# Kernel tuning notes

Hardware: AMD Instinct MI355X
Metric: run time of the kernel (lower is better)

The kernel has to match this reference:

```python
import jax, jax.numpy as jnp
import numpy as np

IN_C = 256
OUT_C = 256
HID = IN_C * 2
N_POINTS = 262144
N_NODES = 8192
B = 16
MAX_NODES = 512
EPS = 1e-5


def _mlp(h, w1, b1, g1, be1, w2, b2):
    # PyG MLP([C, 2C, out], norm='layer_norm'): lin -> layernorm -> relu -> (dropout, eval=identity) -> lin
    h = h @ w1 + b1
    mu = jnp.mean(h, axis=-1, keepdims=True)
    var = jnp.var(h, axis=-1, keepdims=True)
    h = (h - mu) * jax.lax.rsqrt(var + EPS) * g1 + be1
    h = jax.nn.relu(h)
    return h @ w2 + b2


def setup_inputs() -> dict:
    key = jax.random.key(0)
    ks = jax.random.split(key, 16)
    x = jax.random.normal(ks[0], (N_POINTS, IN_C), dtype=jnp.float32)
    f_point_batches = jnp.sort(jax.random.randint(ks[1], (N_POINTS,), 0, N_NODES)).astype(jnp.int32)
    # equal-sized graphs (16 graphs x 512 nodes), sorted as torch.split/pad_sequence assume
    g_node_batches = jnp.repeat(jnp.arange(B, dtype=jnp.int32), MAX_NODES)
    s = 1.0 / np.sqrt(IN_C)
    s2 = 1.0 / np.sqrt(HID)
    def lin(k, fan_in, shape, scale):
        return jax.random.uniform(k, shape, jnp.float32, -scale, scale)
    params = {}
    for i, name in enumerate(['Wq', 'Wk']):
        base = 2 + i * 6
        params[f'{name}_w1'] = lin(ks[base + 0], IN_C, (IN_C, HID), s)
        params[f'{name}_b1'] = lin(ks[base + 1], IN_C, (HID,), s)
        params[f'{name}_g1'] = jnp.ones((HID,), jnp.float32)
        params[f'{name}_be1'] = jnp.zeros((HID,), jnp.float32)
        params[f'{name}_w2'] = lin(ks[base + 2], HID, (HID, OUT_C), s2)
        params[f'{name}_b2'] = lin(ks[base + 3], HID, (OUT_C,), s2)
    return dict(x=x, f_point_batches=f_point_batches, g_node_batches=g_node_batches,
                num_graphs=B, max_nodes=MAX_NODES, **params)


def reference(x, f_point_batches, g_node_batches, num_graphs, max_nodes,
              Wq_w1, Wq_b1, Wq_g1, Wq_be1, Wq_w2, Wq_b2,
              Wk_w1, Wk_b1, Wk_g1, Wk_be1, Wk_w2, Wk_b2):
    n_nodes = g_node_batches.shape[0]
    C = x.shape[1]
    # scatter_mean over points -> per-node feature means [n_nodes, C]
    sums = jax.ops.segment_sum(x, f_point_batches, num_segments=n_nodes)
    cnt = jax.ops.segment_sum(jnp.ones((x.shape[0],), x.dtype), f_point_batches, num_segments=n_nodes)
    mean = sums / jnp.maximum(cnt, 1.0)[:, None]
    # ragged split by graph + pad_sequence -> [B, max_nodes, C]
    starts = jnp.searchsorted(g_node_batches, jnp.arange(num_graphs, dtype=g_node_batches.dtype))
    pos = jnp.arange(n_nodes) - starts[g_node_batches]
    padded = jnp.zeros((num_graphs, max_nodes, C), x.dtype).at[g_node_batches, pos].set(mean, mode='drop')
    q = _mlp(padded, Wq_w1, Wq_b1, Wq_g1, Wq_be1, Wq_w2, Wq_b2)  # [B, MAXN, out]
    k = _mlp(padded, Wk_w1, Wk_b1, Wk_g1, Wk_be1, Wk_w2, Wk_b2)
    return jnp.einsum('bnd,bmd->bnm', q, k)  # bmm(q, k^T)
```

## Files before the change

### kernel.cpp

```cpp
#include <hip/hip_runtime.h>
#include <hip/hip_bf16.h>

#define N_POINTS 262144
#define N_NODES  8192
#define IN_C     256
#define HID      512
#define OUT_C    256
#define NB       16
#define MAXN     512
#define EPSV     1e-5f
#define NPB      32

typedef __attribute__((ext_vector_type(8))) short short8;
typedef __attribute__((ext_vector_type(4))) float f32x4;
typedef __attribute__((ext_vector_type(4))) float f4v;
#define MFMA16(a, b, c) __builtin_amdgcn_mfma_f32_16x16x32_bf16((a), (b), (c), 0, 0, 0)


__global__ __launch_bounds__(256) void prelude_k(
    const int* __restrict__ fpb, int* __restrict__ starts,
    const float* __restrict__ W1q, const float* __restrict__ W1k,
    const float* __restrict__ W2q, const float* __restrict__ W2k,
    __hip_bfloat16* __restrict__ P1q, __hip_bfloat16* __restrict__ P1k,
    __hip_bfloat16* __restrict__ P2q, __hip_bfloat16* __restrict__ P2k)
{
  if (blockIdx.x < 1024) {
    const int i = blockIdx.x * 256 + threadIdx.x;
    const int cur = fpb[i];
    const int prev = (i == 0) ? -1 : fpb[i - 1];
    for (int n = prev + 1; n <= cur; ++n) starts[n] = i;
    if (i == N_POINTS - 1)
      for (int n = cur + 1; n <= N_NODES; ++n) starts[n] = N_POINTS;
    return;
  }
  const int bid = blockIdx.x - 1024;
  const int sel = bid >> 6;
  const float* W; __hip_bfloat16* P; int N;
  switch (sel) {
    case 0:  W = W1q; P = P1q; N = HID;   break;
    case 1:  W = W1k; P = P1k; N = HID;   break;
    case 2:  W = W2q; P = P2q; N = OUT_C; break;
    default: W = W2k; P = P2k; N = OUT_C; break;
  }
  const int idx = (bid & 63) * 256 + threadIdx.x;
  const int NF = N >> 4;
  const int lane = idx & 63;
  const int nf = (idx >> 6) % NF;
  const int ks = idx / (64 * NF);
  const int k0 = ks * 32 + (lane >> 4) * 8;
  const int n  = nf * 16 + (lane & 15);
  __hip_bfloat16 tmp[8];
  #pragma unroll
  for (int j = 0; j < 8; ++j) tmp[j] = __float2bfloat16(W[(size_t)(k0 + j) * N + n]);
  *(uint4*)(P + (size_t)idx * 8) = *(uint4*)tmp;
}

__global__ __launch_bounds__(512, 2) void fused_mlp_k(
    const float* __restrict__ x, const int* __restrict__ starts,
    const __hip_bfloat16* __restrict__ P1q, const __hip_bfloat16* __restrict__ P2q,
    const float* __restrict__ b1q, const float* __restrict__ g1q,
    const float* __restrict__ be1q, const float* __restrict__ b2q,
    const __hip_bfloat16* __restrict__ P1k, const __hip_bfloat16* __restrict__ P2k,
    const float* __restrict__ b1k, const float* __restrict__ g1k,
    const float* __restrict__ be1k, const float* __restrict__ b2k,
    __hip_bfloat16* __restrict__ qo, __hip_bfloat16* __restrict__ ko)
{
  const int n0 = blockIdx.x * NPB;
  const int t = threadIdx.x;
  const int w = t >> 6, l = t & 63, lg = l >> 4, lm = l & 15;
  const int h = w >> 2;
  const int c = w & 3;

  const __hip_bfloat16* P1 = h ? P1k : P1q;
  const __hip_bfloat16* P2 = h ? P2k : P2q;
  const float* b1  = h ? b1k  : b1q;
  const float* g1  = h ? g1k  : g1q;
  const float* be1 = h ? be1k : be1q;
  const float* b2  = h ? b2k  : b2q;
  __hip_bfloat16* out = h ? ko : qo;

  __shared__ __hip_bfloat16 As[NPB * 264];
  __shared__ __hip_bfloat16 Hs[2][NPB * 520];
  __shared__ float lnp[8][NPB][2];

  #pragma unroll
  for (int i = 0; i < 4; ++i) {
    const int nl = w * 4 + i;
    const int node = n0 + nl;
    const int s_ = starts[node], e_ = starts[node + 1];
    const int cnt = e_ - s_;
    f4v a0 = (f4v)0.f, a1 = (f4v)0.f, a2 = (f4v)0.f, a3 = (f4v)0.f, a4 = (f4v)0.f, a5 = (f4v)0.f;
    if (cnt > 0) {
      for (int r = s_; r < e_; r += 6) {
        int i0 = r,     i1 = r + 1, i2 = r + 2, i3 = r + 3, i4 = r + 4, i5 = r + 5;
        int v1ok = i1 < e_, v2ok = i2 < e_, v3ok = i3 < e_, v4ok = i4 < e_, v5ok = i5 < e_;
        i1 = v1ok ? i1 : s_; i2 = v2ok ? i2 : s_; i3 = v3ok ? i3 : s_;
        i4 = v4ok ? i4 : s_; i5 = v5ok ? i5 : s_;
        f4v v0 = __builtin_nontemporal_load((const f4v*)(x + (size_t)i0 * IN_C + l * 4));
        f4v v1 = __builtin_nontemporal_load((const f4v*)(x + (size_t)i1 * IN_C + l * 4));
        f4v v2 = __builtin_nontemporal_load((const f4v*)(x + (size_t)i2 * IN_C + l * 4));
        f4v v3 = __builtin_nontemporal_load((const f4v*)(x + (size_t)i3 * IN_C + l * 4));
        f4v v4 = __builtin_nontemporal_load((const f4v*)(x + (size_t)i4 * IN_C + l * 4));
        f4v v5 = __builtin_nontemporal_load((const f4v*)(x + (size_t)i5 * IN_C + l * 4));
        a0 += v0;
        a1 += v1ok ? v1 : (f4v)0.f;
        a2 += v2ok ? v2 : (f4v)0.f;
        a3 += v3ok ? v3 : (f4v)0.f;
        a4 += v4ok ? v4 : (f4v)0.f;
        a5 += v5ok ? v5 : (f4v)0.f;
      }
    }
    a0 += a1 + a2 + a3 + a4 + a5;
    const float inv = cnt > 0 ? 1.0f / (float)cnt : 0.0f;
    __hip_bfloat16 o[4];
    o[0] = __float2bfloat16(a0.x * inv);
    o[1] = __float2bfloat16(a0.y * inv);
    o[2] = __float2bfloat16(a0.z * inv);
    o[3] = __float2bfloat16(a0.w * inv);
    *(uint2*)(As + nl * 264 + l * 4) = *(uint2*)o;
  }
  __syncthreads();

  f32x4 acc1[2][8];
  #pragma unroll
  for (int mi = 0; mi < 2; ++mi)
    #pragma unroll
    for (int nj = 0; nj < 8; ++nj)
      #pragma unroll
      for (int r = 0; r < 4; ++r) acc1[mi][nj][r] = 0.f;

  for (int ks = 0; ks < 8; ++ks) {
    short8 a0 = *(const short8*)(As + lm * 264 + ks * 32 + lg * 8);
    short8 a1 = *(const short8*)(As + (16 + lm) * 264 + ks * 32 + lg * 8);
    const __hip_bfloat16* bp = P1 + ((size_t)(ks * 32 + c * 8) * 64 + l) * 8;
    #pragma unroll
    for (int nj = 0; nj < 8; ++nj) {
      short8 b = *(const short8*)(bp + (size_t)nj * 512);
      acc1[0][nj] = MFMA16(a0, b, acc1[0][nj]);
      acc1[1][nj] = MFMA16(a1, b, acc1[1][nj]);
    }
  }

  float b1v[8], g1v[8], e1v[8];
  #pragma unroll
  for (int nj = 0; nj < 8; ++nj) {
    const int col = c * 128 + nj * 16 + lm;
    b1v[nj] = b1[col]; g1v[nj] = g1[col]; e1v[nj] = be1[col];
  }
  #pragma unroll
  for (int mi = 0; mi < 2; ++mi)
    #pragma unroll
    for (int nj = 0; nj < 8; ++nj)
      #pragma unroll
      for (int r = 0; r < 4; ++r) acc1[mi][nj][r] += b1v[nj];

  #pragma unroll
  for (int mi = 0; mi < 2; ++mi)
    #pragma unroll
    for (int r = 0; r < 4; ++r) {
      float s = 0.f, q = 0.f;
      #pragma unroll
      for (int nj = 0; nj < 8; ++nj) {
        const float v = acc1[mi][nj][r];
        s += v; q += v * v;
      }
      #pragma unroll
      for (int off = 1; off < 16; off <<= 1) {
        s += __shfl_xor(s, off);
        q += __shfl_xor(q, off);
      }
      if (lm == 0) {
        const int row = mi * 16 + lg * 4 + r;
        lnp[w][row][0] = s;
        lnp[w][row][1] = q;
      }
    }
  __syncthreads();

  #pragma unroll
  for (int mi = 0; mi < 2; ++mi)
    #pragma unroll
    for (int r = 0; r < 4; ++r) {
      const int row = mi * 16 + lg * 4 + r;
      float S = 0.f, Q = 0.f;
      #pragma unroll
      for (int w2 = 0; w2 < 4; ++w2) {
        S += lnp[h * 4 + w2][row][0];
        Q += lnp[h * 4 + w2][row][1];
      }
      const float mu = S * (1.0f / HID);
      const float rs = rsqrtf(Q * (1.0f / HID) - mu * mu + EPSV);
      #pragma unroll
      for (int nj = 0; nj < 8; ++nj) {
        const float y = (acc1[mi][nj][r] - mu) * rs * g1v[nj] + e1v[nj];
        Hs[h][row * 520 + c * 128 + nj * 16 + lm] = __float2bfloat16(fmaxf(y, 0.f));
      }
    }
  __syncthreads();

  f32x4 acc2[2][4];
  #pragma unroll
  for (int mi = 0; mi < 2; ++mi)
    #pragma unroll
    for (int nj = 0; nj < 4; ++nj)
      #pragma unroll
      for (int r = 0; r < 4; ++r) acc2[mi][nj][r] = 0.f;

  for (int ks = 0; ks < 16; ++ks) {
    short8 a0 = *(const short8*)(Hs[h] + lm * 520 + ks * 32 + lg * 8);
    short8 a1 = *(const short8*)(Hs[h] + (16 + lm) * 520 + ks * 32 + lg * 8);
    const __hip_bfloat16* bp = P2 + ((size_t)(ks * 16 + c * 4) * 64 + l) * 8;
    #pragma unroll
    for (int nj = 0; nj < 4; ++nj) {
      short8 b = *(const short8*)(bp + (size_t)nj * 512);
      acc2[0][nj] = MFMA16(a0, b, acc2[0][nj]);
      acc2[1][nj] = MFMA16(a1, b, acc2[1][nj]);
    }
  }

  float b2v[4];
  #pragma unroll
  for (int nj = 0; nj < 4; ++nj) b2v[nj] = b2[c * 64 + nj * 16 + lm];
  #pragma unroll
  for (int mi = 0; mi < 2; ++mi)
    #pragma unroll
    for (int nj = 0; nj < 4; ++nj)
      #pragma unroll
      for (int r = 0; r < 4; ++r) {
        const int row = n0 + mi * 16 + lg * 4 + r;
        const int col = c * 64 + nj * 16 + lm;
        out[(size_t)row * OUT_C + col] = __float2bfloat16(acc2[mi][nj][r] + b2v[nj]);
      }
}

__global__ __launch_bounds__(256, 4) void bmm_k(
    const __hip_bfloat16* __restrict__ q, const __hip_bfloat16* __restrict__ k,
    float* __restrict__ out)
{
  const int b  = blockIdx.z;
  const int n0 = blockIdx.x * 64;
  const int m0 = blockIdx.y * 64;
  const int t = threadIdx.x;
  const int w = t >> 6, l = t & 63, lg = l >> 4, lm = l & 15;

  const __hip_bfloat16* qb = q + ((size_t)b * MAXN + n0 + w * 16) * OUT_C;
  const __hip_bfloat16* kb = k + ((size_t)b * MAXN + m0) * OUT_C;

  f32x4 acc[4];
  #pragma unroll
  for (int nj = 0; nj < 4; ++nj)
    #pragma unroll
    for (int r = 0; r < 4; ++r) acc[nj][r] = 0.f;

  for (int ks = 0; ks < 8; ++ks) {
    short8 a = *(const short8*)(qb + (size_t)lm * OUT_C + ks * 32 + lg * 8);
    #pragma unroll
    for (int nj = 0; nj < 4; ++nj) {
      short8 bb = *(const short8*)(kb + (size_t)(nj * 16 + lm) * OUT_C + ks * 32 + lg * 8);
      acc[nj] = MFMA16(a, bb, acc[nj]);
    }
  }

  #pragma unroll
  for (int nj = 0; nj < 4; ++nj)
    #pragma unroll
    for (int r = 0; r < 4; ++r) {
      const int nrow = n0 + w * 16 + lg * 4 + r;
      const int mcol = m0 + nj * 16 + lm;
      out[((size_t)b * MAXN + nrow) * MAXN + mcol] = acc[nj][r];
    }
}

extern "C" void kernel_launch(void* const* d_in, const int* in_sizes, int n_in,
                              void* d_out, int out_size, void* d_ws, size_t ws_size,
                              hipStream_t stream)
{
  const float* x   = (const float*)d_in[0];
  const int*   fpb = (const int*)d_in[1];
  const float* Wq_w1  = (const float*)d_in[5];
  const float* Wq_b1  = (const float*)d_in[6];
  const float* Wq_g1  = (const float*)d_in[7];
  const float* Wq_be1 = (const float*)d_in[8];
  const float* Wq_w2  = (const float*)d_in[9];
  const float* Wq_b2  = (const float*)d_in[10];
  const float* Wk_w1  = (const float*)d_in[11];
  const float* Wk_b1  = (const float*)d_in[12];
  const float* Wk_g1  = (const float*)d_in[13];
  const float* Wk_be1 = (const float*)d_in[14];
  const float* Wk_w2  = (const float*)d_in[15];
  const float* Wk_b2  = (const float*)d_in[16];

  __hip_bfloat16* ws = (__hip_bfloat16*)d_ws;
  __hip_bfloat16* P1q  = ws;
  __hip_bfloat16* P1k  = P1q + 131072;
  __hip_bfloat16* P2q  = P1k + 131072;
  __hip_bfloat16* P2k  = P2q + 131072;
  __hip_bfloat16* qo   = P2k + 131072;
  __hip_bfloat16* ko   = qo + 2097152;
  int* starts = (int*)(ko + 2097152);
  float* out = (float*)d_out;

  prelude_k<<<1280, 256, 0, stream>>>(fpb, starts,
      Wq_w1, Wk_w1, Wq_w2, Wk_w2, P1q, P1k, P2q, P2k);
  fused_mlp_k<<<N_NODES / NPB, 512, 0, stream>>>(
      x, starts, P1q, P2q, Wq_b1, Wq_g1, Wq_be1, Wq_b2,
      P1k, P2k, Wk_b1, Wk_g1, Wk_be1, Wk_b2, qo, ko);
  bmm_k<<<dim3(8, 8, NB), 256, 0, stream>>>(qo, ko, out);
}
```

Before: 92.66 us.

## Serialize Q and K MLP heads across all waves to raise occupancy

Instead of splitting the 8 waves into a Q group and a K group, all 8 waves now process the Q MLP and then the K MLP in sequence. Each wave holds half as many accumulators and the block keeps only one hidden buffer in shared memory, and the launch bound goes from 2 to 4 blocks per CU. The scatter-mean loop is also rewritten as a plain 4-way unrolled loop with a scalar tail, replacing the 6-way predicated non-temporal loads. In exchange the MLP phases run serially, with extra barriers and a second pass of the layernorm reduction.

```diff
diff --git a/kernel.cpp b/kernel.cpp
--- a/kernel.cpp
+++ b/kernel.cpp
@@ -55,7 +55,23 @@
   *(uint4*)(P + (size_t)idx * 8) = *(uint4*)tmp;
 }
 
-__global__ __launch_bounds__(512, 2) void fused_mlp_k(
+__device__ __forceinline__ void accum_rows(
+    const float* __restrict__ x, int lo, int hi, int l,
+    f4v& a0, f4v& a1, f4v& a2, f4v& a3)
+{
+  int r = lo;
+  for (; r + 4 <= hi; r += 4) {
+    f4v v0 = *(const f4v*)(x + (size_t)(r + 0) * IN_C + l * 4);
+    f4v v1 = *(const f4v*)(x + (size_t)(r + 1) * IN_C + l * 4);
+    f4v v2 = *(const f4v*)(x + (size_t)(r + 2) * IN_C + l * 4);
+    f4v v3 = *(const f4v*)(x + (size_t)(r + 3) * IN_C + l * 4);
+    a0 += v0; a1 += v1; a2 += v2; a3 += v3;
+  }
+  for (; r < hi; ++r)
+    a0 += *(const f4v*)(x + (size_t)r * IN_C + l * 4);
+}
+
+__global__ __launch_bounds__(512, 4) void fused_mlp_k(
     const float* __restrict__ x, const int* __restrict__ starts,
     const __hip_bfloat16* __restrict__ P1q, const __hip_bfloat16* __restrict__ P2q,
     const float* __restrict__ b1q, const float* __restrict__ g1q,
@@ -68,19 +84,9 @@
   const int n0 = blockIdx.x * NPB;
   const int t = threadIdx.x;
   const int w = t >> 6, l = t & 63, lg = l >> 4, lm = l & 15;
-  const int h = w >> 2;
-  const int c = w & 3;
-
-  const __hip_bfloat16* P1 = h ? P1k : P1q;
-  const __hip_bfloat16* P2 = h ? P2k : P2q;
-  const float* b1  = h ? b1k  : b1q;
-  const float* g1  = h ? g1k  : g1q;
-  const float* be1 = h ? be1k : be1q;
-  const float* b2  = h ? b2k  : b2q;
-  __hip_bfloat16* out = h ? ko : qo;
 
   __shared__ __hip_bfloat16 As[NPB * 264];
-  __shared__ __hip_bfloat16 Hs[2][NPB * 520];
+  __shared__ __hip_bfloat16 Hs[NPB * 520];
   __shared__ float lnp[8][NPB][2];
 
   #pragma unroll
@@ -88,29 +94,10 @@
     const int nl = w * 4 + i;
     const int node = n0 + nl;
     const int s_ = starts[node], e_ = starts[node + 1];
+    f4v a0 = (f4v)0.f, a1 = (f4v)0.f, a2 = (f4v)0.f, a3 = (f4v)0.f;
+    accum_rows(x, s_, e_, l, a0, a1, a2, a3);
+    a0 += a1 + a2 + a3;
     const int cnt = e_ - s_;
-    f4v a0 = (f4v)0.f, a1 = (f4v)0.f, a2 = (f4v)0.f, a3 = (f4v)0.f, a4 = (f4v)0.f, a5 = (f4v)0.f;
-    if (cnt > 0) {
-      for (int r = s_; r < e_; r += 6) {
-        int i0 = r,     i1 = r + 1, i2 = r + 2, i3 = r + 3, i4 = r + 4, i5 = r + 5;
-        int v1ok = i1 < e_, v2ok = i2 < e_, v3ok = i3 < e_, v4ok = i4 < e_, v5ok = i5 < e_;
-        i1 = v1ok ? i1 : s_; i2 = v2ok ? i2 : s_; i3 = v3ok ? i3 : s_;
-        i4 = v4ok ? i4 : s_; i5 = v5ok ? i5 : s_;
-        f4v v0 = __builtin_nontemporal_load((const f4v*)(x + (size_t)i0 * IN_C + l * 4));
-        f4v v1 = __builtin_nontemporal_load((const f4v*)(x + (size_t)i1 * IN_C + l * 4));
-        f4v v2 = __builtin_nontemporal_load((const f4v*)(x + (size_t)i2 * IN_C + l * 4));
-        f4v v3 = __builtin_nontemporal_load((const f4v*)(x + (size_t)i3 * IN_C + l * 4));
-        f4v v4 = __builtin_nontemporal_load((const f4v*)(x + (size_t)i4 * IN_C + l * 4));
-        f4v v5 = __builtin_nontemporal_load((const f4v*)(x + (size_t)i5 * IN_C + l * 4));
-        a0 += v0;
-        a1 += v1ok ? v1 : (f4v)0.f;
-        a2 += v2ok ? v2 : (f4v)0.f;
-        a3 += v3ok ? v3 : (f4v)0.f;
-        a4 += v4ok ? v4 : (f4v)0.f;
-        a5 += v5ok ? v5 : (f4v)0.f;
-      }
-    }
-    a0 += a1 + a2 + a3 + a4 + a5;
     const float inv = cnt > 0 ? 1.0f / (float)cnt : 0.0f;
     __hip_bfloat16 o[4];
     o[0] = __float2bfloat16(a0.x * inv);
@@ -121,116 +108,127 @@
   }
   __syncthreads();
 
-  f32x4 acc1[2][8];
-  #pragma unroll
-  for (int mi = 0; mi < 2; ++mi)
-    #pragma unroll
-    for (int nj = 0; nj < 8; ++nj)
-      #pragma unroll
-      for (int r = 0; r < 4; ++r) acc1[mi][nj][r] = 0.f;
-
-  for (int ks = 0; ks < 8; ++ks) {
-    short8 a0 = *(const short8*)(As + lm * 264 + ks * 32 + lg * 8);
-    short8 a1 = *(const short8*)(As + (16 + lm) * 264 + ks * 32 + lg * 8);
-    const __hip_bfloat16* bp = P1 + ((size_t)(ks * 32 + c * 8) * 64 + l) * 8;
-    #pragma unroll
-    for (int nj = 0; nj < 8; ++nj) {
-      short8 b = *(const short8*)(bp + (size_t)nj * 512);
-      acc1[0][nj] = MFMA16(a0, b, acc1[0][nj]);
-      acc1[1][nj] = MFMA16(a1, b, acc1[1][nj]);
-    }
-  }
-
-  float b1v[8], g1v[8], e1v[8];
-  #pragma unroll
-  for (int nj = 0; nj < 8; ++nj) {
-    const int col = c * 128 + nj * 16 + lm;
-    b1v[nj] = b1[col]; g1v[nj] = g1[col]; e1v[nj] = be1[col];
-  }
-  #pragma unroll
-  for (int mi = 0; mi < 2; ++mi)
-    #pragma unroll
-    for (int nj = 0; nj < 8; ++nj)
-      #pragma unroll
-      for (int r = 0; r < 4; ++r) acc1[mi][nj][r] += b1v[nj];
-
-  #pragma unroll
-  for (int mi = 0; mi < 2; ++mi)
-    #pragma unroll
-    for (int r = 0; r < 4; ++r) {
-      float s = 0.f, q = 0.f;
-      #pragma unroll
-      for (int nj = 0; nj < 8; ++nj) {
-        const float v = acc1[mi][nj][r];
-        s += v; q += v * v;
+  for (int hh = 0; hh < 2; ++hh) {
+    const __hip_bfloat16* P1 = hh ? P1k : P1q;
+    const __hip_bfloat16* P2 = hh ? P2k : P2q;
+    const float* b1  = hh ? b1k  : b1q;
+    const float* g1  = hh ? g1k  : g1q;
+    const float* be1 = hh ? be1k : be1q;
+    const float* b2  = hh ? b2k  : b2q;
+    __hip_bfloat16* out = hh ? ko : qo;
+
+    f32x4 acc1[2][4];
+    #pragma unroll
+    for (int mi = 0; mi < 2; ++mi)
+      #pragma unroll
+      for (int nj = 0; nj < 4; ++nj)
+        #pragma unroll
+        for (int r = 0; r < 4; ++r) acc1[mi][nj][r] = 0.f;
+
+    for (int ks = 0; ks < 8; ++ks) {
+      short8 a0 = *(const short8*)(As + lm * 264 + ks * 32 + lg * 8);
+      short8 a1 = *(const short8*)(As + (16 + lm) * 264 + ks * 32 + lg * 8);
+      const __hip_bfloat16* bp = P1 + ((size_t)(ks * 32 + w * 4) * 64 + l) * 8;
+      #pragma unroll
+      for (int nj = 0; nj < 4; ++nj) {
+        short8 b = *(const short8*)(bp + (size_t)nj * 512);
+        acc1[0][nj] = MFMA16(a0, b, acc1[0][nj]);
+        acc1[1][nj] = MFMA16(a1, b, acc1[1][nj]);
       }
-      #pragma unroll
-      for (int off = 1; off < 16; off <<= 1) {
-        s += __shfl_xor(s, off);
-        q += __shfl_xor(q, off);
+    }
+
+    float b1v[4], g1v[4], e1v[4];
+    #pragma unroll
+    for (int nj = 0; nj < 4; ++nj) {
+      const int col = w * 64 + nj * 16 + lm;
+      b1v[nj] = b1[col]; g1v[nj] = g1[col]; e1v[nj] = be1[col];
+    }
+    #pragma unroll
+    for (int mi = 0; mi < 2; ++mi)
+      #pragma unroll
+      for (int nj = 0; nj < 4; ++nj)
+        #pragma unroll
+        for (int r = 0; r < 4; ++r) acc1[mi][nj][r] += b1v[nj];
+
+    #pragma unroll
+    for (int mi = 0; mi < 2; ++mi)
+      #pragma unroll
+      for (int r = 0; r < 4; ++r) {
+        float s = 0.f, q = 0.f;
+        #pragma unroll
+        for (int nj = 0; nj < 4; ++nj) {
+          const float v = acc1[mi][nj][r];
+          s += v; q += v * v;
+        }
+        #pragma unroll
+        for (int off = 1; off < 16; off <<= 1) {
+          s += __shfl_xor(s, off);
+          q += __shfl_xor(q, off);
+        }
+        if (lm == 0) {
+          const int row = mi * 16 + lg * 4 + r;
+          lnp[w][row][0] = s;
+          lnp[w][row][1] = q;
+        }
       }
-      if (lm == 0) {
+    __syncthreads();
+
+    #pragma unroll
+    for (int mi = 0; mi < 2; ++mi)
+      #pragma unroll
+      for (int r = 0; r < 4; ++r) {
         const int row = mi * 16 + lg * 4 + r;
-        lnp[w][row][0] = s;
-        lnp[w][row][1] = q;
+        float S = 0.f, Q = 0.f;
+        #pragma unroll
+        for (int w2 = 0; w2 < 8; ++w2) {
+          S += lnp[w2][row][0];
+          Q += lnp[w2][row][1];
+        }
+        const float mu = S * (1.0f / HID);
+        const float rs = rsqrtf(Q * (1.0f / HID) - mu * mu + EPSV);
+        #pragma unroll
+        for (int nj = 0; nj < 4; ++nj) {
+          const float y = (acc1[mi][nj][r] - mu) * rs * g1v[nj] + e1v[nj];
+          Hs[row * 520 + w * 64 + nj * 16 + lm] = __float2bfloat16(fmaxf(y, 0.f));
+        }
       }
-    }
-  __syncthreads();
-
-  #pragma unroll
-  for (int mi = 0; mi < 2; ++mi)
-    #pragma unroll
-    for (int r = 0; r < 4; ++r) {
-      const int row = mi * 16 + lg * 4 + r;
-      float S = 0.f, Q = 0.f;
-      #pragma unroll
-      for (int w2 = 0; w2 < 4; ++w2) {
-        S += lnp[h * 4 + w2][row][0];
-        Q += lnp[h * 4 + w2][row][1];
+    __syncthreads();
+
+    f32x4 acc2[2][2];
+    #pragma unroll
+    for (int mi = 0; mi < 2; ++mi)
+      #pragma unroll
+      for (int nj = 0; nj < 2; ++nj)
+        #pragma unroll
+        for (int r = 0; r < 4; ++r) acc2[mi][nj][r] = 0.f;
+
+    for (int ks = 0; ks < 16; ++ks) {
+      short8 a0 = *(const short8*)(Hs + lm * 520 + ks * 32 + lg * 8);
+      short8 a1 = *(const short8*)(Hs + (16 + lm) * 520 + ks * 32 + lg * 8);
+      const __hip_bfloat16* bp = P2 + ((size_t)(ks * 16 + w * 2) * 64 + l) * 8;
+      #pragma unroll
+      for (int nj = 0; nj < 2; ++nj) {
+        short8 b = *(const short8*)(bp + (size_t)nj * 512);
+        acc2[0][nj] = MFMA16(a0, b, acc2[0][nj]);
+        acc2[1][nj] = MFMA16(a1, b, acc2[1][nj]);
       }
-      const float mu = S * (1.0f / HID);
-      const float rs = rsqrtf(Q * (1.0f / HID) - mu * mu + EPSV);
-      #pragma unroll
-      for (int nj = 0; nj < 8; ++nj) {
-        const float y = (acc1[mi][nj][r] - mu) * rs * g1v[nj] + e1v[nj];
-        Hs[h][row * 520 + c * 128 + nj * 16 + lm] = __float2bfloat16(fmaxf(y, 0.f));
-      }
-    }
-  __syncthreads();
-
-  f32x4 acc2[2][4];
-  #pragma unroll
-  for (int mi = 0; mi < 2; ++mi)
-    #pragma unroll
-    for (int nj = 0; nj < 4; ++nj)
-      #pragma unroll
-      for (int r = 0; r < 4; ++r) acc2[mi][nj][r] = 0.f;
-
-  for (int ks = 0; ks < 16; ++ks) {
-    short8 a0 = *(const short8*)(Hs[h] + lm * 520 + ks * 32 + lg * 8);
-    short8 a1 = *(const short8*)(Hs[h] + (16 + lm) * 520 + ks * 32 + lg * 8);
-    const __hip_bfloat16* bp = P2 + ((size_t)(ks * 16 + c * 4) * 64 + l) * 8;
-    #pragma unroll
-    for (int nj = 0; nj < 4; ++nj) {
-      short8 b = *(const short8*)(bp + (size_t)nj * 512);
-      acc2[0][nj] = MFMA16(a0, b, acc2[0][nj]);
-      acc2[1][nj] = MFMA16(a1, b, acc2[1][nj]);
-    }
-  }
-
-  float b2v[4];
-  #pragma unroll
-  for (int nj = 0; nj < 4; ++nj) b2v[nj] = b2[c * 64 + nj * 16 + lm];
-  #pragma unroll
-  for (int mi = 0; mi < 2; ++mi)
-    #pragma unroll
-    for (int nj = 0; nj < 4; ++nj)
-      #pragma unroll
-      for (int r = 0; r < 4; ++r) {
-        const int row = n0 + mi * 16 + lg * 4 + r;
-        const int col = c * 64 + nj * 16 + lm;
-        out[(size_t)row * OUT_C + col] = __float2bfloat16(acc2[mi][nj][r] + b2v[nj]);
-      }
+    }
+
+    float b2v[2];
+    #pragma unroll
+    for (int nj = 0; nj < 2; ++nj) b2v[nj] = b2[w * 32 + nj * 16 + lm];
+    #pragma unroll
+    for (int mi = 0; mi < 2; ++mi)
+      #pragma unroll
+      for (int nj = 0; nj < 2; ++nj)
+        #pragma unroll
+        for (int r = 0; r < 4; ++r) {
+          const int row = n0 + mi * 16 + lg * 4 + r;
+          const int col = w * 32 + nj * 16 + lm;
+          out[(size_t)row * OUT_C + col] = __float2bfloat16(acc2[mi][nj][r] + b2v[nj]);
+        }
+    __syncthreads();
+  }
 }
 
 __global__ __launch_bounds__(256, 4) void bmm_k(
```

Result: slower. 96.19 us (+3.8%).

## Alias input tile into hidden buffer and raise occupancy of fused MLP kernel

Applied to the files above, without the earlier changes.

Removes the separate As shared buffer by aliasing it onto the second hidden-activation buffer, which lowers shared memory per block. Launch bounds go from 2 to 4 blocks per SM so more waves can run concurrently. The scatter-mean accumulation loop is rewritten as a clean 4-way unrolled loop with a scalar tail and plain loads instead of the masked 6-way nontemporal loads. Risks: the tighter register budget may cause spills, and the aliasing depends on As being fully consumed by the first GEMM before Hs1 is written.

```diff
diff --git a/kernel.cpp b/kernel.cpp
--- a/kernel.cpp
+++ b/kernel.cpp
@@ -55,7 +55,23 @@
   *(uint4*)(P + (size_t)idx * 8) = *(uint4*)tmp;
 }
 
-__global__ __launch_bounds__(512, 2) void fused_mlp_k(
+__device__ __forceinline__ void accum_rows(
+    const float* __restrict__ x, int lo, int hi, int l,
+    f4v& a0, f4v& a1, f4v& a2, f4v& a3)
+{
+  int r = lo;
+  for (; r + 4 <= hi; r += 4) {
+    f4v v0 = *(const f4v*)(x + (size_t)(r + 0) * IN_C + l * 4);
+    f4v v1 = *(const f4v*)(x + (size_t)(r + 1) * IN_C + l * 4);
+    f4v v2 = *(const f4v*)(x + (size_t)(r + 2) * IN_C + l * 4);
+    f4v v3 = *(const f4v*)(x + (size_t)(r + 3) * IN_C + l * 4);
+    a0 += v0; a1 += v1; a2 += v2; a3 += v3;
+  }
+  for (; r < hi; ++r)
+    a0 += *(const f4v*)(x + (size_t)r * IN_C + l * 4);
+}
+
+__global__ __launch_bounds__(512, 4) void fused_mlp_k(
     const float* __restrict__ x, const int* __restrict__ starts,
     const __hip_bfloat16* __restrict__ P1q, const __hip_bfloat16* __restrict__ P2q,
     const float* __restrict__ b1q, const float* __restrict__ g1q,
@@ -79,38 +95,22 @@
   const float* b2  = h ? b2k  : b2q;
   __hip_bfloat16* out = h ? ko : qo;
 
-  __shared__ __hip_bfloat16 As[NPB * 264];
-  __shared__ __hip_bfloat16 Hs[2][NPB * 520];
+  __shared__ __hip_bfloat16 HsBuf[2 * NPB * 520];
   __shared__ float lnp[8][NPB][2];
+  __hip_bfloat16* Hs0 = HsBuf;
+  __hip_bfloat16* Hs1 = HsBuf + NPB * 520;
+  __hip_bfloat16* As  = Hs1;
+  __hip_bfloat16* Hsh = h ? Hs1 : Hs0;
 
   #pragma unroll
   for (int i = 0; i < 4; ++i) {
     const int nl = w * 4 + i;
     const int node = n0 + nl;
     const int s_ = starts[node], e_ = starts[node + 1];
+    f4v a0 = (f4v)0.f, a1 = (f4v)0.f, a2 = (f4v)0.f, a3 = (f4v)0.f;
+    accum_rows(x, s_, e_, l, a0, a1, a2, a3);
+    a0 += a1 + a2 + a3;
     const int cnt = e_ - s_;
-    f4v a0 = (f4v)0.f, a1 = (f4v)0.f, a2 = (f4v)0.f, a3 = (f4v)0.f, a4 = (f4v)0.f, a5 = (f4v)0.f;
-    if (cnt > 0) {
-      for (int r = s_; r < e_; r += 6) {
-        int i0 = r,     i1 = r + 1, i2 = r + 2, i3 = r + 3, i4 = r + 4, i5 = r + 5;
-        int v1ok = i1 < e_, v2ok = i2 < e_, v3ok = i3 < e_, v4ok = i4 < e_, v5ok = i5 < e_;
-        i1 = v1ok ? i1 : s_; i2 = v2ok ? i2 : s_; i3 = v3ok ? i3 : s_;
-        i4 = v4ok ? i4 : s_; i5 = v5ok ? i5 : s_;
-        f4v v0 = __builtin_nontemporal_load((const f4v*)(x + (size_t)i0 * IN_C + l * 4));
-        f4v v1 = __builtin_nontemporal_load((const f4v*)(x + (size_t)i1 * IN_C + l * 4));
-        f4v v2 = __builtin_nontemporal_load((const f4v*)(x + (size_t)i2 * IN_C + l * 4));
-        f4v v3 = __builtin_nontemporal_load((const f4v*)(x + (size_t)i3 * IN_C + l * 4));
-        f4v v4 = __builtin_nontemporal_load((const f4v*)(x + (size_t)i4 * IN_C + l * 4));
-        f4v v5 = __builtin_nontemporal_load((const f4v*)(x + (size_t)i5 * IN_C + l * 4));
-        a0 += v0;
-        a1 += v1ok ? v1 : (f4v)0.f;
-        a2 += v2ok ? v2 : (f4v)0.f;
-        a3 += v3ok ? v3 : (f4v)0.f;
-        a4 += v4ok ? v4 : (f4v)0.f;
-        a5 += v5ok ? v5 : (f4v)0.f;
-      }
-    }
-    a0 += a1 + a2 + a3 + a4 + a5;
     const float inv = cnt > 0 ? 1.0f / (float)cnt : 0.0f;
     __hip_bfloat16 o[4];
     o[0] = __float2bfloat16(a0.x * inv);
@@ -193,7 +193,7 @@
       #pragma unroll
       for (int nj = 0; nj < 8; ++nj) {
         const float y = (acc1[mi][nj][r] - mu) * rs * g1v[nj] + e1v[nj];
-        Hs[h][row * 520 + c * 128 + nj * 16 + lm] = __float2bfloat16(fmaxf(y, 0.f));
+        Hsh[row * 520 + c * 128 + nj * 16 + lm] = __float2bfloat16(fmaxf(y, 0.f));
       }
     }
   __syncthreads();
@@ -207,8 +207,8 @@
       for (int r = 0; r < 4; ++r) acc2[mi][nj][r] = 0.f;
 
   for (int ks = 0; ks < 16; ++ks) {
-    short8 a0 = *(const short8*)(Hs[h] + lm * 520 + ks * 32 + lg * 8);
-    short8 a1 = *(const short8*)(Hs[h] + (16 + lm) * 520 + ks * 32 + lg * 8);
+    short8 a0 = *(const short8*)(Hsh + lm * 520 + ks * 32 + lg * 8);
+    short8 a1 = *(const short8*)(Hsh + (16 + lm) * 520 + ks * 32 + lg * 8);
     const __hip_bfloat16* bp = P2 + ((size_t)(ks * 16 + c * 4) * 64 + l) * 8;
     #pragma unroll
     for (int nj = 0; nj < 4; ++nj) {
```

After: 103.6 us. 11.8% more time.
